# Performance work log

Measured on AMD Instinct MI355X. Metric: run time of the kernel, lower is better.

Reference implementation:

```python
import jax, jax.numpy as jnp
import numpy as np

N_NODES = 100000
N_EDGES = 3200000
D_IN = 256
D_OUT = 256


def setup_inputs() -> dict:
    key = jax.random.key(0)
    k1, k2, k3, k4, k5 = jax.random.split(key, 5)
    x = jax.random.normal(k1, (N_NODES, D_IN), dtype=jnp.float32)
    # xavier-uniform-like init for weight
    limit = float(np.sqrt(6.0 / (D_IN + D_OUT)))
    weight = jax.random.uniform(k2, (D_IN, D_OUT), dtype=jnp.float32, minval=-limit, maxval=limit)
    edge_val = jax.random.uniform(k3, (N_EDGES,), dtype=jnp.float32)
    edge_row = jax.random.randint(k4, (N_EDGES,), 0, N_NODES, dtype=jnp.int32)
    edge_col = jax.random.randint(k5, (N_EDGES,), 0, N_NODES, dtype=jnp.int32)
    return {"x": x, "weight": weight, "edge_val": edge_val,
            "edge_row": edge_row, "edge_col": edge_col}


def reference(x, weight, edge_val, edge_row, edge_col):
    # dropout p=0.0 -> identity
    support = x @ weight                                  # [N, D_OUT]
    # spmm: out[r] += val * support[c] for each edge (r, c, val)
    msgs = support[edge_col] * edge_val[:, None]          # [E, D_OUT]
    out = jax.ops.segment_sum(msgs, edge_row, num_segments=N_NODES)
    return jax.nn.relu(out)
```

## Files before the change

### kernel.cpp

```cpp
#include <hip/hip_runtime.h>

#define N_NODES 100000
#define N_EDGES 3200000
#define D 256
#define CAP 64
#define OVF_MAX 8192

#define NB1 98
#define RPB1 1024
#define CAPB1 34816
#define CHUNK 6144
#define NBLK_A ((N_EDGES + CHUNK - 1) / CHUNK)

#define CAST_BLOCKS 6250
#define GEMM_BLOCKS (N_NODES / 16)

typedef __attribute__((ext_vector_type(8))) short bf16x8;
typedef __attribute__((ext_vector_type(4))) float f32x4;

__device__ unsigned short g_wtp[(size_t)16 * 8 * 64 * 8];
__device__ int   g_cursor[N_NODES];
__device__ int   g_b1cur[NB1];
__device__ int   g_novf;
__device__ int   g_ovf_row[OVF_MAX];
__device__ int2  g_ovf_edge[OVF_MAX];

__device__ unsigned short g_xb_fb[(size_t)N_NODES * D];
__device__ unsigned       g_y_fb[(size_t)N_NODES * (D / 2)];
__device__ int2           g_pad_fb[(size_t)N_NODES * CAP];
__device__ int2           g_binned_fb[(size_t)NB1 * CAPB1];

__device__ __forceinline__ unsigned short f2bf(float f) {
    unsigned u = __float_as_uint(f);
    unsigned r = u + 0x7fffu + ((u >> 16) & 1u);
    return (unsigned short)(r >> 16);
}

__global__ void setup_kernel(const float* __restrict__ W) {
    const int tid = threadIdx.x;
    if (blockIdx.x < 64) {
        int pb = (blockIdx.x * 256 + tid) * 4;
        #pragma unroll
        for (int j = 0; j < 4; ++j) {
            int p    = pb + j;
            int i8   = p & 7;
            int lane = (p >> 3) & 63;
            int s    = (p >> 9) & 7;
            int nt   = p >> 12;
            int n = nt * 16 + (lane & 15);
            int k = s * 32 + (lane >> 4) * 8 + i8;
            g_wtp[p] = f2bf(W[(size_t)k * D + n]);
        }
    }
    if (blockIdx.x == 0) {
        if (tid < NB1) g_b1cur[tid] = 0;
        if (tid == 0) g_novf = 0;
    }
}

__launch_bounds__(256)
__global__ void binA_kernel(const float* __restrict__ edge_val,
                            const int* __restrict__ edge_row,
                            const int* __restrict__ edge_col,
                            int2* __restrict__ binned) {
    __shared__ int2 rec[CHUNK];
    __shared__ unsigned char bid[CHUNK];
    __shared__ int cnt[NB1];
    __shared__ int pre[NB1 + 1];
    __shared__ int bas[NB1];
    const int tid = threadIdx.x;
    const int e0 = blockIdx.x * CHUNK;

    for (int k = tid; k < NB1; k += 256) cnt[k] = 0;
    __syncthreads();
    #pragma unroll
    for (int j = 0; j < CHUNK / 256; ++j) {
        int e = e0 + tid + j * 256;
        if (e < N_EDGES) atomicAdd(&cnt[edge_row[e] >> 10], 1);
    }
    __syncthreads();
    if (tid == 0) {
        int run = 0;
        for (int k = 0; k < NB1; ++k) { pre[k] = run; run += cnt[k]; }
        pre[NB1] = run;
    }
    __syncthreads();
    for (int k = tid; k < NB1; k += 256)
        bas[k] = cnt[k] ? atomicAdd(&g_b1cur[k], cnt[k]) : 0;
    __syncthreads();
    for (int k = tid; k < NB1; k += 256) cnt[k] = 0;
    __syncthreads();
    #pragma unroll
    for (int j = 0; j < CHUNK / 256; ++j) {
        int e = e0 + tid + j * 256;
        if (e < N_EDGES) {
            int r = edge_row[e];
            int k = r >> 10;
            int o = atomicAdd(&cnt[k], 1);
            int pos = pre[k] + o;
            int2 pk;
            pk.x = edge_col[e] | ((r & 1023) << 17);
            pk.y = __float_as_int(edge_val[e]);
            rec[pos] = pk;
            bid[pos] = (unsigned char)k;
        }
    }
    __syncthreads();
    const int total = pre[NB1];
    for (int i = tid; i < total; i += 256) {
        int k = bid[i];
        int dest = bas[k] + (i - pre[k]);
        int2 pk = rec[i];
        if (dest < CAPB1) {
            binned[(size_t)k * CAPB1 + dest] = pk;
        } else {
            int o = atomicAdd(&g_novf, 1);
            if (o < OVF_MAX) {
                g_ovf_row[o] = (k << 10) | (pk.x >> 17);
                int2 ov; ov.x = pk.x & 0x1FFFF; ov.y = pk.y;
                g_ovf_edge[o] = ov;
            }
        }
    }
}

__launch_bounds__(256)
__global__ void binB_cast_kernel(const float* __restrict__ x,
                                 const int2* __restrict__ binned,
                                 int2* __restrict__ pad,
                                 unsigned short* __restrict__ xb) {
    __shared__ int cur[RPB1];
    const int tid = threadIdx.x;
    const int b = blockIdx.x;

    if (b < NB1) {
        for (int i = tid; i < RPB1; i += 256) cur[i] = 0;
        __syncthreads();
        const int n = min(g_b1cur[b], CAPB1);
        const int2* src = &binned[(size_t)b * CAPB1];
        for (int i = tid; i < n; i += 256) {
            int2 pk = src[i];
            int rl  = pk.x >> 17;
            int col = pk.x & 0x1FFFF;
            int slot = atomicAdd(&cur[rl], 1);
            int row = (b << 10) + rl;
            int2 o2; o2.x = col; o2.y = pk.y;
            if (slot < CAP) {
                pad[(size_t)row * CAP + slot] = o2;
            } else {
                int o = atomicAdd(&g_novf, 1);
                if (o < OVF_MAX) { g_ovf_row[o] = row; g_ovf_edge[o] = o2; }
            }
        }
        __syncthreads();
        for (int i = tid; i < RPB1; i += 256) {
            int row = (b << 10) + i;
            if (row < N_NODES) g_cursor[row] = cur[i];
        }
    } else {
        const size_t blockBase = (size_t)(b - NB1) * 4096;
        #pragma unroll
        for (int j = 0; j < 4; ++j) {
            size_t idx = blockBase + (size_t)(j * 256 + tid) * 4;
            float4 f = *(const float4*)&x[idx];
            unsigned short o[4];
            o[0] = f2bf(f.x); o[1] = f2bf(f.y);
            o[2] = f2bf(f.z); o[3] = f2bf(f.w);
            *(uint2*)&xb[idx] = *(const uint2*)o;
        }
    }
}

__launch_bounds__(128)
__global__ void spmm_kernel(const int2* __restrict__ pad,
                            const unsigned short* __restrict__ xbp,
                            unsigned* __restrict__ y) {
    const int r = blockIdx.x;
    const int t = threadIdx.x;
    const int deg = g_cursor[r];
    const int dpad = min(deg, CAP);
    const long long* rowp = (const long long*)&pad[(size_t)r * CAP];
    const unsigned* xb = (const unsigned*)xbp;

    float a0 = 0.f, a1 = 0.f;
    int i = 0;
    for (; i + 3 < dpad; i += 4) {
        long long q0 = __builtin_nontemporal_load(&rowp[i]);
        long long q1 = __builtin_nontemporal_load(&rowp[i + 1]);
        long long q2 = __builtin_nontemporal_load(&rowp[i + 2]);
        long long q3 = __builtin_nontemporal_load(&rowp[i + 3]);
        unsigned p0 = xb[(size_t)(int)q0 * (D / 2) + t];
        unsigned p1 = xb[(size_t)(int)q1 * (D / 2) + t];
        unsigned p2 = xb[(size_t)(int)q2 * (D / 2) + t];
        unsigned p3 = xb[(size_t)(int)q3 * (D / 2) + t];
        float v0 = __int_as_float((int)(q0 >> 32));
        float v1 = __int_as_float((int)(q1 >> 32));
        float v2 = __int_as_float((int)(q2 >> 32));
        float v3 = __int_as_float((int)(q3 >> 32));
        a0 += v0 * __uint_as_float(p0 << 16);
        a1 += v0 * __uint_as_float(p0 & 0xffff0000u);
        a0 += v1 * __uint_as_float(p1 << 16);
        a1 += v1 * __uint_as_float(p1 & 0xffff0000u);
        a0 += v2 * __uint_as_float(p2 << 16);
        a1 += v2 * __uint_as_float(p2 & 0xffff0000u);
        a0 += v3 * __uint_as_float(p3 << 16);
        a1 += v3 * __uint_as_float(p3 & 0xffff0000u);
    }
    for (; i < dpad; ++i) {
        long long q0 = __builtin_nontemporal_load(&rowp[i]);
        float v0 = __int_as_float((int)(q0 >> 32));
        unsigned p0 = xb[(size_t)(int)q0 * (D / 2) + t];
        a0 += v0 * __uint_as_float(p0 << 16);
        a1 += v0 * __uint_as_float(p0 & 0xffff0000u);
    }
    const int novf = min(g_novf, OVF_MAX);
    if (novf > 0) {
        for (int j = 0; j < novf; ++j) {
            if (g_ovf_row[j] == r) {
                int2 e0 = g_ovf_edge[j];
                float v0 = __int_as_float(e0.y);
                unsigned p0 = xb[(size_t)e0.x * (D / 2) + t];
                a0 += v0 * __uint_as_float(p0 << 16);
                a1 += v0 * __uint_as_float(p0 & 0xffff0000u);
            }
        }
    }
    y[(size_t)r * (D / 2) + t] =
        (unsigned)f2bf(a0) | ((unsigned)f2bf(a1) << 16);
}

__launch_bounds__(256)
__global__ void gemm_kernel(const unsigned short* __restrict__ Yb,
                            float* __restrict__ out) {
    __shared__ float tile[4][16][68];
    const int g    = blockIdx.x;
    const int wave = threadIdx.x >> 6;
    const int lane = threadIdx.x & 63;
    const int m0   = g * 16;
    const int n0   = wave * 64;
    const int lm   = lane & 15;
    const int q    = lane >> 4;

    f32x4 acc0 = {}, acc1 = {}, acc2 = {}, acc3 = {};

    #pragma unroll
    for (int s = 0; s < 8; ++s) {
        bf16x8 av = *(const bf16x8*)&Yb[(size_t)(m0 + lm) * D + s * 32 + q * 8];
        const unsigned short* bp =
            &g_wtp[((size_t)(wave * 4) * 8 + s) * 512 + lane * 8];
        bf16x8 b0 = *(const bf16x8*)&bp[0 * 4096];
        bf16x8 b1 = *(const bf16x8*)&bp[1 * 4096];
        bf16x8 b2 = *(const bf16x8*)&bp[2 * 4096];
        bf16x8 b3 = *(const bf16x8*)&bp[3 * 4096];
        acc0 = __builtin_amdgcn_mfma_f32_16x16x32_bf16(av, b0, acc0, 0, 0, 0);
        acc1 = __builtin_amdgcn_mfma_f32_16x16x32_bf16(av, b1, acc1, 0, 0, 0);
        acc2 = __builtin_amdgcn_mfma_f32_16x16x32_bf16(av, b2, acc2, 0, 0, 0);
        acc3 = __builtin_amdgcn_mfma_f32_16x16x32_bf16(av, b3, acc3, 0, 0, 0);
    }

    #pragma unroll
    for (int r = 0; r < 4; ++r) {
        tile[wave][q * 4 + r][ 0 + lm] = acc0[r];
        tile[wave][q * 4 + r][16 + lm] = acc1[r];
        tile[wave][q * 4 + r][32 + lm] = acc2[r];
        tile[wave][q * 4 + r][48 + lm] = acc3[r];
    }
    const int row  = lane >> 2;
    const int cseg = (lane & 3) * 16;
    float ov[16];
    #pragma unroll
    for (int j = 0; j < 16; ++j)
        ov[j] = fmaxf(tile[wave][row][cseg + j], 0.f);
    float* dst = &out[(size_t)(m0 + row) * D + n0 + cseg];
    #pragma unroll
    for (int j = 0; j < 4; ++j)
        __builtin_nontemporal_store(*(const f32x4*)&ov[j * 4], (f32x4*)&dst[j * 4]);
}

#define XB_BYTES   ((size_t)N_NODES * D * 2)
#define Y_BYTES    ((size_t)N_NODES * D * 2)
#define PAD_BYTES  ((size_t)N_NODES * CAP * 8)
#define BIN_BYTES  ((size_t)NB1 * CAPB1 * 8)
#define ALIGNUP(v) (((v) + 255) & ~(size_t)255)

extern "C" void kernel_launch(void* const* d_in, const int* in_sizes, int n_in,
                              void* d_out, int out_size, void* d_ws, size_t ws_size,
                              hipStream_t stream) {
    const float* x        = (const float*)d_in[0];
    const float* weight   = (const float*)d_in[1];
    const float* edge_val = (const float*)d_in[2];
    const int*   edge_row = (const int*)d_in[3];
    const int*   edge_col = (const int*)d_in[4];
    float* out = (float*)d_out;

    static void* s_xb = nullptr; static void* s_y = nullptr;
    static void* s_pad = nullptr; static void* s_bin = nullptr;
    if (!s_xb) {
        hipGetSymbolAddress(&s_xb,  HIP_SYMBOL(g_xb_fb));
        hipGetSymbolAddress(&s_y,   HIP_SYMBOL(g_y_fb));
        hipGetSymbolAddress(&s_pad, HIP_SYMBOL(g_pad_fb));
        hipGetSymbolAddress(&s_bin, HIP_SYMBOL(g_binned_fb));
    }
    unsigned short* xb;  unsigned* y;  int2* pad;  int2* binned;
    const size_t need = ALIGNUP(XB_BYTES) + ALIGNUP(Y_BYTES) +
                        ALIGNUP(PAD_BYTES) + ALIGNUP(BIN_BYTES);
    if (d_ws && ws_size >= need) {
        char* p = (char*)d_ws;
        xb     = (unsigned short*)p; p += ALIGNUP(XB_BYTES);
        y      = (unsigned*)p;       p += ALIGNUP(Y_BYTES);
        pad    = (int2*)p;           p += ALIGNUP(PAD_BYTES);
        binned = (int2*)p;
    } else {
        xb     = (unsigned short*)s_xb;
        y      = (unsigned*)s_y;
        pad    = (int2*)s_pad;
        binned = (int2*)s_bin;
    }

    setup_kernel<<<64, 256, 0, stream>>>(weight);
    binA_kernel<<<NBLK_A, 256, 0, stream>>>(edge_val, edge_row, edge_col, binned);
    binB_cast_kernel<<<NB1 + CAST_BLOCKS, 256, 0, stream>>>(x, binned, pad, xb);
    spmm_kernel<<<N_NODES, 128, 0, stream>>>(pad, xb, y);
    gemm_kernel<<<GEMM_BLOCKS, 256, 0, stream>>>((const unsigned short*)y, out);
}
```

Measured before the change: 623.6 us.

## Fuse second binning pass into SpMM via LDS-resident per-row edge lists

```diff
diff --git a/kernel.cpp b/kernel.cpp
--- a/kernel.cpp
+++ b/kernel.cpp
@@ -12,6 +12,9 @@
 #define CHUNK 6144
 #define NBLK_A ((N_EDGES + CHUNK - 1) / CHUNK)
 
+#define SLICES 8
+#define RPS 128
+
 #define CAST_BLOCKS 6250
 #define GEMM_BLOCKS (N_NODES / 16)
 
@@ -19,7 +22,6 @@
 typedef __attribute__((ext_vector_type(4))) float f32x4;
 
 __device__ unsigned short g_wtp[(size_t)16 * 8 * 64 * 8];
-__device__ int   g_cursor[N_NODES];
 __device__ int   g_b1cur[NB1];
 __device__ int   g_novf;
 __device__ int   g_ovf_row[OVF_MAX];
@@ -27,7 +29,6 @@
 
 __device__ unsigned short g_xb_fb[(size_t)N_NODES * D];
 __device__ unsigned       g_y_fb[(size_t)N_NODES * (D / 2)];
-__device__ int2           g_pad_fb[(size_t)N_NODES * CAP];
 __device__ int2           g_binned_fb[(size_t)NB1 * CAPB1];
 
 __device__ __forceinline__ unsigned short f2bf(float f) {
@@ -59,106 +60,75 @@
 }
 
 __launch_bounds__(256)
-__global__ void binA_kernel(const float* __restrict__ edge_val,
-                            const int* __restrict__ edge_row,
-                            const int* __restrict__ edge_col,
-                            int2* __restrict__ binned) {
+__global__ void binA_cast_kernel(const float* __restrict__ x,
+                                 const float* __restrict__ edge_val,
+                                 const int* __restrict__ edge_row,
+                                 const int* __restrict__ edge_col,
+                                 int2* __restrict__ binned,
+                                 unsigned short* __restrict__ xb) {
     __shared__ int2 rec[CHUNK];
     __shared__ unsigned char bid[CHUNK];
     __shared__ int cnt[NB1];
     __shared__ int pre[NB1 + 1];
     __shared__ int bas[NB1];
     const int tid = threadIdx.x;
-    const int e0 = blockIdx.x * CHUNK;
-
-    for (int k = tid; k < NB1; k += 256) cnt[k] = 0;
-    __syncthreads();
-    #pragma unroll
-    for (int j = 0; j < CHUNK / 256; ++j) {
-        int e = e0 + tid + j * 256;
-        if (e < N_EDGES) atomicAdd(&cnt[edge_row[e] >> 10], 1);
-    }
-    __syncthreads();
-    if (tid == 0) {
-        int run = 0;
-        for (int k = 0; k < NB1; ++k) { pre[k] = run; run += cnt[k]; }
-        pre[NB1] = run;
-    }
-    __syncthreads();
-    for (int k = tid; k < NB1; k += 256)
-        bas[k] = cnt[k] ? atomicAdd(&g_b1cur[k], cnt[k]) : 0;
-    __syncthreads();
-    for (int k = tid; k < NB1; k += 256) cnt[k] = 0;
-    __syncthreads();
-    #pragma unroll
-    for (int j = 0; j < CHUNK / 256; ++j) {
-        int e = e0 + tid + j * 256;
-        if (e < N_EDGES) {
-            int r = edge_row[e];
-            int k = r >> 10;
-            int o = atomicAdd(&cnt[k], 1);
-            int pos = pre[k] + o;
-            int2 pk;
-            pk.x = edge_col[e] | ((r & 1023) << 17);
-            pk.y = __float_as_int(edge_val[e]);
-            rec[pos] = pk;
-            bid[pos] = (unsigned char)k;
-        }
-    }
-    __syncthreads();
-    const int total = pre[NB1];
-    for (int i = tid; i < total; i += 256) {
-        int k = bid[i];
-        int dest = bas[k] + (i - pre[k]);
-        int2 pk = rec[i];
-        if (dest < CAPB1) {
-            binned[(size_t)k * CAPB1 + dest] = pk;
-        } else {
-            int o = atomicAdd(&g_novf, 1);
-            if (o < OVF_MAX) {
-                g_ovf_row[o] = (k << 10) | (pk.x >> 17);
-                int2 ov; ov.x = pk.x & 0x1FFFF; ov.y = pk.y;
-                g_ovf_edge[o] = ov;
+    const int b = blockIdx.x;
+
+    if (b < NBLK_A) {
+        const int e0 = b * CHUNK;
+        for (int k = tid; k < NB1; k += 256) cnt[k] = 0;
+        __syncthreads();
+        #pragma unroll
+        for (int j = 0; j < CHUNK / 256; ++j) {
+            int e = e0 + tid + j * 256;
+            if (e < N_EDGES) atomicAdd(&cnt[edge_row[e] >> 10], 1);
+        }
+        __syncthreads();
+        if (tid == 0) {
+            int run = 0;
+            for (int k = 0; k < NB1; ++k) { pre[k] = run; run += cnt[k]; }
+            pre[NB1] = run;
+        }
+        __syncthreads();
+        for (int k = tid; k < NB1; k += 256)
+            bas[k] = cnt[k] ? atomicAdd(&g_b1cur[k], cnt[k]) : 0;
+        __syncthreads();
+        for (int k = tid; k < NB1; k += 256) cnt[k] = 0;
+        __syncthreads();
+        #pragma unroll
+        for (int j = 0; j < CHUNK / 256; ++j) {
+            int e = e0 + tid + j * 256;
+            if (e < N_EDGES) {
+                int r = edge_row[e];
+                int k = r >> 10;
+                int o = atomicAdd(&cnt[k], 1);
+                int pos = pre[k] + o;
+                int2 pk;
+                pk.x = edge_col[e] | ((r & 1023) << 17);
+                pk.y = __float_as_int(edge_val[e]);
+                rec[pos] = pk;
+                bid[pos] = (unsigned char)k;
             }
         }
-    }
-}
-
-__launch_bounds__(256)
-__global__ void binB_cast_kernel(const float* __restrict__ x,
-                                 const int2* __restrict__ binned,
-                                 int2* __restrict__ pad,
-                                 unsigned short* __restrict__ xb) {
-    __shared__ int cur[RPB1];
-    const int tid = threadIdx.x;
-    const int b = blockIdx.x;
-
-    if (b < NB1) {
-        for (int i = tid; i < RPB1; i += 256) cur[i] = 0;
-        __syncthreads();
-        const int n = min(g_b1cur[b], CAPB1);
-        const int2* src = &binned[(size_t)b * CAPB1];
-        for (int i = tid; i < n; i += 256) {
-            int2 pk = src[i];
-            int rl  = pk.x >> 17;
-            int col = pk.x & 0x1FFFF;
-            int slot = atomicAdd(&cur[rl], 1);
-            int row = (b << 10) + rl;
-            int2 o2; o2.x = col; o2.y = pk.y;
-            if (slot < CAP) {
-                pad[(size_t)row * CAP + slot] = o2;
+        __syncthreads();
+        const int total = pre[NB1];
+        for (int i = tid; i < total; i += 256) {
+            int k = bid[i];
+            int dest = bas[k] + (i - pre[k]);
+            int2 pk = rec[i];
+            if (dest < CAPB1) {
+                binned[(size_t)k * CAPB1 + dest] = pk;
             } else {
                 int o = atomicAdd(&g_novf, 1);
-                if (o < OVF_MAX) { g_ovf_row[o] = row; g_ovf_edge[o] = o2; }
+                if (o < OVF_MAX) {
+                    g_ovf_row[o] = (k << 10) | (pk.x >> 17);
+                    int2 ov; ov.x = pk.x & 0x1FFFF; ov.y = pk.y;
+                    g_ovf_edge[o] = ov;
+                }
             }
         }
-        __syncthreads();
-        for (int i = tid; i < RPB1; i += 256) {
-            int row = (b << 10) + i;
-            if (row < N_NODES) g_cursor[row] = cur[i];
-        }
     } else {
-        const size_t blockBase = (size_t)(b - NB1) * 4096;
+        const size_t blockBase = (size_t)(b - NBLK_A) * 4096;
         #pragma unroll
         for (int j = 0; j < 4; ++j) {
             size_t idx = blockBase + (size_t)(j * 256 + tid) * 4;
@@ -171,62 +141,98 @@
     }
 }
 
-__launch_bounds__(128)
-__global__ void spmm_kernel(const int2* __restrict__ pad,
-                            const unsigned short* __restrict__ xbp,
-                            unsigned* __restrict__ y) {
-    const int r = blockIdx.x;
-    const int t = threadIdx.x;
-    const int deg = g_cursor[r];
-    const int dpad = min(deg, CAP);
-    const long long* rowp = (const long long*)&pad[(size_t)r * CAP];
+__launch_bounds__(256)
+__global__ void bin_spmm_kernel(const int2* __restrict__ binned,
+                                const unsigned short* __restrict__ xbp,
+                                unsigned* __restrict__ y) {
+    __shared__ int2 pad[RPS * CAP];
+    __shared__ int cur[RPS];
+    const int tid   = threadIdx.x;
+    const int bkt   = blockIdx.x >> 3;
+    const int slice = blockIdx.x & 7;
+
+    const int n = min(g_b1cur[bkt], CAPB1);
+    const int2* src = &binned[(size_t)bkt * CAPB1];
+
+    if (tid < RPS) cur[tid] = 0;
+    __syncthreads();
+    for (int i = tid; i < n; i += 256) {
+        int2 pk = src[i];
+        int rl = pk.x >> 17;
+        if ((rl >> 7) == slice) {
+            int rl7 = rl & 127;
+            int slot = atomicAdd(&cur[rl7], 1);
+            int2 o2; o2.x = pk.x & 0x1FFFF; o2.y = pk.y;
+            if (slot < CAP) {
+                pad[(rl7 << 6) + slot] = o2;
+            } else {
+                int o = atomicAdd(&g_novf, 1);
+                if (o < OVF_MAX) {
+                    g_ovf_row[o] = (bkt << 10) + (slice << 7) + rl7;
+                    g_ovf_edge[o] = o2;
+                }
+            }
+        }
+    }
+    __syncthreads();
+
+    const int grp = tid >> 7;
+    const int t   = tid & 127;
     const unsigned* xb = (const unsigned*)xbp;
-
-    float a0 = 0.f, a1 = 0.f;
-    int i = 0;
-    for (; i + 3 < dpad; i += 4) {
-        long long q0 = __builtin_nontemporal_load(&rowp[i]);
-        long long q1 = __builtin_nontemporal_load(&rowp[i + 1]);
-        long long q2 = __builtin_nontemporal_load(&rowp[i + 2]);
-        long long q3 = __builtin_nontemporal_load(&rowp[i + 3]);
-        unsigned p0 = xb[(size_t)(int)q0 * (D / 2) + t];
-        unsigned p1 = xb[(size_t)(int)q1 * (D / 2) + t];
-        unsigned p2 = xb[(size_t)(int)q2 * (D / 2) + t];
-        unsigned p3 = xb[(size_t)(int)q3 * (D / 2) + t];
-        float v0 = __int_as_float((int)(q0 >> 32));
-        float v1 = __int_as_float((int)(q1 >> 32));
-        float v2 = __int_as_float((int)(q2 >> 32));
-        float v3 = __int_as_float((int)(q3 >> 32));
-        a0 += v0 * __uint_as_float(p0 << 16);
-        a1 += v0 * __uint_as_float(p0 & 0xffff0000u);
-        a0 += v1 * __uint_as_float(p1 << 16);
-        a1 += v1 * __uint_as_float(p1 & 0xffff0000u);
-        a0 += v2 * __uint_as_float(p2 << 16);
-        a1 += v2 * __uint_as_float(p2 & 0xffff0000u);
-        a0 += v3 * __uint_as_float(p3 << 16);
-        a1 += v3 * __uint_as_float(p3 & 0xffff0000u);
-    }
-    for (; i < dpad; ++i) {
-        long long q0 = __builtin_nontemporal_load(&rowp[i]);
-        float v0 = __int_as_float((int)(q0 >> 32));
-        unsigned p0 = xb[(size_t)(int)q0 * (D / 2) + t];
-        a0 += v0 * __uint_as_float(p0 << 16);
-        a1 += v0 * __uint_as_float(p0 & 0xffff0000u);
-    }
     const int novf = min(g_novf, OVF_MAX);
-    if (novf > 0) {
-        for (int j = 0; j < novf; ++j) {
-            if (g_ovf_row[j] == r) {
-                int2 e0 = g_ovf_edge[j];
-                float v0 = __int_as_float(e0.y);
-                unsigned p0 = xb[(size_t)e0.x * (D / 2) + t];
-                a0 += v0 * __uint_as_float(p0 << 16);
-                a1 += v0 * __uint_as_float(p0 & 0xffff0000u);
+
+    for (int rp = 0; rp < RPS / 2; ++rp) {
+        const int rl7 = rp * 2 + grp;
+        const int row = (bkt << 10) + (slice << 7) + rl7;
+        if (row >= N_NODES) continue;
+        const int deg = min(cur[rl7], CAP);
+        const int2* prow = &pad[rl7 << 6];
+        float a0 = 0.f, a1 = 0.f;
+        int i = 0;
+        for (; i + 3 < deg; i += 4) {
+            int2 e0 = prow[i];
+            int2 e1 = prow[i + 1];
+            int2 e2 = prow[i + 2];
+            int2 e3 = prow[i + 3];
+            unsigned p0 = xb[(size_t)e0.x * (D / 2) + t];
+            unsigned p1 = xb[(size_t)e1.x * (D / 2) + t];
+            unsigned p2 = xb[(size_t)e2.x * (D / 2) + t];
+            unsigned p3 = xb[(size_t)e3.x * (D / 2) + t];
+            float v0 = __int_as_float(e0.y);
+            float v1 = __int_as_float(e1.y);
+            float v2 = __int_as_float(e2.y);
+            float v3 = __int_as_float(e3.y);
+            a0 += v0 * __uint_as_float(p0 << 16);
+            a1 += v0 * __uint_as_float(p0 & 0xffff0000u);
+            a0 += v1 * __uint_as_float(p1 << 16);
+            a1 += v1 * __uint_as_float(p1 & 0xffff0000u);
+            a0 += v2 * __uint_as_float(p2 << 16);
+            a1 += v2 * __uint_as_float(p2 & 0xffff0000u);
+            a0 += v3 * __uint_as_float(p3 << 16);
+            a1 += v3 * __uint_as_float(p3 & 0xffff0000u);
+        }
+        for (; i < deg; ++i) {
+            int2 e0 = prow[i];
+            unsigned p0 = xb[(size_t)e0.x * (D / 2) + t];
+            float v0 = __int_as_float(e0.y);
+            a0 += v0 * __uint_as_float(p0 << 16);
+            a1 += v0 * __uint_as_float(p0 & 0xffff0000u);
+        }
+        if (novf > 0) {
+            for (int j = 0; j < novf; ++j) {
+                if (g_ovf_row[j] == row) {
+                    int2 ee = g_ovf_edge[j];
+                    float v0 = __int_as_float(ee.y);
+                    unsigned p0 = xb[(size_t)ee.x * (D / 2) + t];
+                    a0 += v0 * __uint_as_float(p0 << 16);
+                    a1 += v0 * __uint_as_float(p0 & 0xffff0000u);
+                }
             }
         }
-    }
-    y[(size_t)r * (D / 2) + t] =
-        (unsigned)f2bf(a0) | ((unsigned)f2bf(a1) << 16);
+        __builtin_nontemporal_store(
+            (unsigned)f2bf(a0) | ((unsigned)f2bf(a1) << 16),
+            &y[(size_t)row * (D / 2) + t]);
+    }
 }
 
 __launch_bounds__(256)
@@ -279,7 +285,6 @@
 
 #define XB_BYTES   ((size_t)N_NODES * D * 2)
 #define Y_BYTES    ((size_t)N_NODES * D * 2)
-#define PAD_BYTES  ((size_t)N_NODES * CAP * 8)
 #define BIN_BYTES  ((size_t)NB1 * CAPB1 * 8)
 #define ALIGNUP(v) (((v) + 255) & ~(size_t)255)
 
@@ -294,32 +299,28 @@
     float* out = (float*)d_out;
 
     static void* s_xb = nullptr; static void* s_y = nullptr;
-    static void* s_pad = nullptr; static void* s_bin = nullptr;
+    static void* s_bin = nullptr;
     if (!s_xb) {
         hipGetSymbolAddress(&s_xb,  HIP_SYMBOL(g_xb_fb));
         hipGetSymbolAddress(&s_y,   HIP_SYMBOL(g_y_fb));
-        hipGetSymbolAddress(&s_pad, HIP_SYMBOL(g_pad_fb));
         hipGetSymbolAddress(&s_bin, HIP_SYMBOL(g_binned_fb));
     }
-    unsigned short* xb;  unsigned* y;  int2* pad;  int2* binned;
-    const size_t need = ALIGNUP(XB_BYTES) + ALIGNUP(Y_BYTES) +
-                        ALIGNUP(PAD_BYTES) + ALIGNUP(BIN_BYTES);
+    unsigned short* xb;  unsigned* y;  int2* binned;
+    const size_t need = ALIGNUP(XB_BYTES) + ALIGNUP(Y_BYTES) + ALIGNUP(BIN_BYTES);
     if (d_ws && ws_size >= need) {
         char* p = (char*)d_ws;
         xb     = (unsigned short*)p; p += ALIGNUP(XB_BYTES);
         y      = (unsigned*)p;       p += ALIGNUP(Y_BYTES);
-        pad    = (int2*)p;           p += ALIGNUP(PAD_BYTES);
         binned = (int2*)p;
     } else {
         xb     = (unsigned short*)s_xb;
         y      = (unsigned*)s_y;
-        pad    = (int2*)s_pad;
         binned = (int2*)s_bin;
     }
 
     setup_kernel<<<64, 256, 0, stream>>>(weight);
-    binA_kernel<<<NBLK_A, 256, 0, stream>>>(edge_val, edge_row, edge_col, binned);
-    binB_cast_kernel<<<NB1 + CAST_BLOCKS, 256, 0, stream>>>(x, binned, pad, xb);
-    spmm_kernel<<<N_NODES, 128, 0, stream>>>(pad, xb, y);
+    binA_cast_kernel<<<NBLK_A + CAST_BLOCKS, 256, 0, stream>>>(
+        x, edge_val, edge_row, edge_col, binned, xb);
+    bin_spmm_kernel<<<NB1 * SLICES, 256, 0, stream>>>(binned, xb, y);
     gemm_kernel<<<GEMM_BLOCKS, 256, 0, stream>>>((const unsigned short*)y, out);
 }
```

New measurement: 930.2 us. 1.49x slower.

## Replace padded per-row edge slots with compact CSR groups sorted in shared memory

Applied to the files above, without the earlier changes.

```diff
diff --git a/kernel.cpp b/kernel.cpp
--- a/kernel.cpp
+++ b/kernel.cpp
@@ -3,32 +3,35 @@
 #define N_NODES 100000
 #define N_EDGES 3200000
 #define D 256
-#define CAP 64
 #define OVF_MAX 8192
 
 #define NB1 98
-#define RPB1 1024
 #define CAPB1 34816
 #define CHUNK 6144
 #define NBLK_A ((N_EDGES + CHUNK - 1) / CHUNK)
 
+#define NQ (NB1 * 4)
+#define QROWS 256
+#define QCAP 9216
+
 #define CAST_BLOCKS 6250
 #define GEMM_BLOCKS (N_NODES / 16)
+#define SPMM_HALF 50000
 
 typedef __attribute__((ext_vector_type(8))) short bf16x8;
 typedef __attribute__((ext_vector_type(4))) float f32x4;
 
 __device__ unsigned short g_wtp[(size_t)16 * 8 * 64 * 8];
-__device__ int   g_cursor[N_NODES];
-__device__ int   g_b1cur[NB1];
+__device__ int   g_b1cur[NB1 * 16];
 __device__ int   g_novf;
 __device__ int   g_ovf_row[OVF_MAX];
 __device__ int2  g_ovf_edge[OVF_MAX];
 
 __device__ unsigned short g_xb_fb[(size_t)N_NODES * D];
 __device__ unsigned       g_y_fb[(size_t)N_NODES * (D / 2)];
-__device__ int2           g_pad_fb[(size_t)N_NODES * CAP];
 __device__ int2           g_binned_fb[(size_t)NB1 * CAPB1];
+__device__ int2           g_grp_fb[(size_t)NQ * QCAP];
+__device__ int2           g_rofs_fb[(size_t)NQ * QROWS];
 
 __device__ __forceinline__ unsigned short f2bf(float f) {
     unsigned u = __float_as_uint(f);
@@ -53,7 +56,7 @@
         }
     }
     if (blockIdx.x == 0) {
-        if (tid < NB1) g_b1cur[tid] = 0;
+        for (int i = tid; i < NB1 * 16; i += 256) g_b1cur[i] = 0;
         if (tid == 0) g_novf = 0;
     }
 }
@@ -86,7 +89,7 @@
     }
     __syncthreads();
     for (int k = tid; k < NB1; k += 256)
-        bas[k] = cnt[k] ? atomicAdd(&g_b1cur[k], cnt[k]) : 0;
+        bas[k] = cnt[k] ? atomicAdd(&g_b1cur[k * 16], cnt[k]) : 0;
     __syncthreads();
     for (int k = tid; k < NB1; k += 256) cnt[k] = 0;
     __syncthreads();
@@ -124,67 +127,98 @@
     }
 }
 
-__launch_bounds__(256)
-__global__ void binB_cast_kernel(const float* __restrict__ x,
-                                 const int2* __restrict__ binned,
-                                 int2* __restrict__ pad,
-                                 unsigned short* __restrict__ xb) {
-    __shared__ int cur[RPB1];
+__launch_bounds__(512)
+__global__ void binB_sort_kernel(const int2* __restrict__ binned,
+                                 int2* __restrict__ grp,
+                                 int2* __restrict__ rofs) {
+    __shared__ int2 srec[QCAP];
+    __shared__ int cnt[QROWS];
+    __shared__ int ofs[QROWS];
+    __shared__ int cur[QROWS];
     const int tid = threadIdx.x;
-    const int b = blockIdx.x;
-
-    if (b < NB1) {
-        for (int i = tid; i < RPB1; i += 256) cur[i] = 0;
-        __syncthreads();
-        const int n = min(g_b1cur[b], CAPB1);
-        const int2* src = &binned[(size_t)b * CAPB1];
-        for (int i = tid; i < n; i += 256) {
-            int2 pk = src[i];
-            int rl  = pk.x >> 17;
-            int col = pk.x & 0x1FFFF;
-            int slot = atomicAdd(&cur[rl], 1);
-            int row = (b << 10) + rl;
-            int2 o2; o2.x = col; o2.y = pk.y;
-            if (slot < CAP) {
-                pad[(size_t)row * CAP + slot] = o2;
+    const int b   = blockIdx.x >> 2;
+    const int qtr = blockIdx.x & 3;
+
+    const int n = min(g_b1cur[b * 16], CAPB1);
+    const int2* src = &binned[(size_t)b * CAPB1];
+
+    if (tid < QROWS) { cnt[tid] = 0; cur[tid] = 0; }
+    __syncthreads();
+    for (int i = tid; i < n; i += 512) {
+        int rl = src[i].x >> 17;
+        if ((rl >> 8) == qtr) atomicAdd(&cnt[rl & 255], 1);
+    }
+    __syncthreads();
+    if (tid < QROWS) {
+        int s = 0;
+        for (int j = 0; j < tid; ++j) s += cnt[j];
+        ofs[tid] = s;
+    }
+    __syncthreads();
+    for (int i = tid; i < n; i += 512) {
+        int2 pk = src[i];
+        int rl = pk.x >> 17;
+        if ((rl >> 8) == qtr) {
+            int r8 = rl & 255;
+            int p = ofs[r8] + atomicAdd(&cur[r8], 1);
+            int2 o2; o2.x = pk.x & 0x1FFFF; o2.y = pk.y;
+            if (p < QCAP) {
+                srec[p] = o2;
             } else {
                 int o = atomicAdd(&g_novf, 1);
-                if (o < OVF_MAX) { g_ovf_row[o] = row; g_ovf_edge[o] = o2; }
+                if (o < OVF_MAX) {
+                    g_ovf_row[o] = (b << 10) + (qtr << 8) + r8;
+                    g_ovf_edge[o] = o2;
+                }
             }
         }
-        __syncthreads();
-        for (int i = tid; i < RPB1; i += 256) {
-            int row = (b << 10) + i;
-            if (row < N_NODES) g_cursor[row] = cur[i];
-        }
-    } else {
-        const size_t blockBase = (size_t)(b - NB1) * 4096;
-        #pragma unroll
-        for (int j = 0; j < 4; ++j) {
-            size_t idx = blockBase + (size_t)(j * 256 + tid) * 4;
-            float4 f = *(const float4*)&x[idx];
-            unsigned short o[4];
-            o[0] = f2bf(f.x); o[1] = f2bf(f.y);
-            o[2] = f2bf(f.z); o[3] = f2bf(f.w);
-            *(uint2*)&xb[idx] = *(const uint2*)o;
-        }
+    }
+    __syncthreads();
+    const int total = min(ofs[QROWS - 1] + cnt[QROWS - 1], QCAP);
+    int2* dst = &grp[(size_t)blockIdx.x * QCAP];
+    for (int i = tid; i < total; i += 512) dst[i] = srec[i];
+    if (tid < QROWS) {
+        int s = min(ofs[tid], QCAP);
+        int e = min(ofs[tid] + cnt[tid], QCAP);
+        int2 oc; oc.x = s; oc.y = e - s;
+        rofs[(size_t)blockIdx.x * QROWS + tid] = oc;
+    }
+}
+
+__launch_bounds__(256)
+__global__ void cast_kernel(const float* __restrict__ x,
+                            unsigned short* __restrict__ xb) {
+    const size_t blockBase = (size_t)blockIdx.x * 4096;
+    const int tid = threadIdx.x;
+    #pragma unroll
+    for (int j = 0; j < 4; ++j) {
+        size_t idx = blockBase + (size_t)(j * 256 + tid) * 4;
+        float4 f = *(const float4*)&x[idx];
+        unsigned short o[4];
+        o[0] = f2bf(f.x); o[1] = f2bf(f.y);
+        o[2] = f2bf(f.z); o[3] = f2bf(f.w);
+        *(uint2*)&xb[idx] = *(const uint2*)o;
     }
 }
 
 __launch_bounds__(128)
-__global__ void spmm_kernel(const int2* __restrict__ pad,
+__global__ void spmm_kernel(const int2* __restrict__ grp,
+                            const int2* __restrict__ rofs,
                             const unsigned short* __restrict__ xbp,
-                            unsigned* __restrict__ y) {
-    const int r = blockIdx.x;
+                            unsigned* __restrict__ y,
+                            int rowBase) {
+    const int r = rowBase + blockIdx.x;
     const int t = threadIdx.x;
-    const int deg = g_cursor[r];
-    const int dpad = min(deg, CAP);
-    const long long* rowp = (const long long*)&pad[(size_t)r * CAP];
+    const int blk = r >> 8;
+    const int2 oc = rofs[(size_t)blk * QROWS + (r & 255)];
+    const int deg = oc.y;
+    const long long* rowp =
+        (const long long*)&grp[(size_t)blk * QCAP + oc.x];
     const unsigned* xb = (const unsigned*)xbp;
 
     float a0 = 0.f, a1 = 0.f;
     int i = 0;
-    for (; i + 3 < dpad; i += 4) {
+    for (; i + 3 < deg; i += 4) {
         long long q0 = __builtin_nontemporal_load(&rowp[i]);
         long long q1 = __builtin_nontemporal_load(&rowp[i + 1]);
         long long q2 = __builtin_nontemporal_load(&rowp[i + 2]);
@@ -206,7 +240,7 @@
         a0 += v3 * __uint_as_float(p3 << 16);
         a1 += v3 * __uint_as_float(p3 & 0xffff0000u);
     }
-    for (; i < dpad; ++i) {
+    for (; i < deg; ++i) {
         long long q0 = __builtin_nontemporal_load(&rowp[i]);
         float v0 = __int_as_float((int)(q0 >> 32));
         unsigned p0 = xb[(size_t)(int)q0 * (D / 2) + t];
@@ -279,8 +313,9 @@
 
 #define XB_BYTES   ((size_t)N_NODES * D * 2)
 #define Y_BYTES    ((size_t)N_NODES * D * 2)
-#define PAD_BYTES  ((size_t)N_NODES * CAP * 8)
 #define BIN_BYTES  ((size_t)NB1 * CAPB1 * 8)
+#define GRP_BYTES  ((size_t)NQ * QCAP * 8)
+#define ROFS_BYTES ((size_t)NQ * QROWS * 8)
 #define ALIGNUP(v) (((v) + 255) & ~(size_t)255)
 
 extern "C" void kernel_launch(void* const* d_in, const int* in_sizes, int n_in,
@@ -294,32 +329,39 @@
     float* out = (float*)d_out;
 
     static void* s_xb = nullptr; static void* s_y = nullptr;
-    static void* s_pad = nullptr; static void* s_bin = nullptr;
+    static void* s_bin = nullptr; static void* s_grp = nullptr;
+    static void* s_rofs = nullptr;
     if (!s_xb) {
-        hipGetSymbolAddress(&s_xb,  HIP_SYMBOL(g_xb_fb));
-        hipGetSymbolAddress(&s_y,   HIP_SYMBOL(g_y_fb));
-        hipGetSymbolAddress(&s_pad, HIP_SYMBOL(g_pad_fb));
-        hipGetSymbolAddress(&s_bin, HIP_SYMBOL(g_binned_fb));
-    }
-    unsigned short* xb;  unsigned* y;  int2* pad;  int2* binned;
+        hipGetSymbolAddress(&s_xb,   HIP_SYMBOL(g_xb_fb));
+        hipGetSymbolAddress(&s_y,    HIP_SYMBOL(g_y_fb));
+        hipGetSymbolAddress(&s_bin,  HIP_SYMBOL(g_binned_fb));
+        hipGetSymbolAddress(&s_grp,  HIP_SYMBOL(g_grp_fb));
+        hipGetSymbolAddress(&s_rofs, HIP_SYMBOL(g_rofs_fb));
+    }
+    unsigned short* xb;  unsigned* y;  int2* binned;  int2* grp;  int2* rofs;
     const size_t need = ALIGNUP(XB_BYTES) + ALIGNUP(Y_BYTES) +
-                        ALIGNUP(PAD_BYTES) + ALIGNUP(BIN_BYTES);
+                        ALIGNUP(BIN_BYTES) + ALIGNUP(GRP_BYTES) +
+                        ALIGNUP(ROFS_BYTES);
     if (d_ws && ws_size >= need) {
         char* p = (char*)d_ws;
         xb     = (unsigned short*)p; p += ALIGNUP(XB_BYTES);
         y      = (unsigned*)p;       p += ALIGNUP(Y_BYTES);
-        pad    = (int2*)p;           p += ALIGNUP(PAD_BYTES);
-        binned = (int2*)p;
+        binned = (int2*)p;           p += ALIGNUP(BIN_BYTES);
+        grp    = (int2*)p;           p += ALIGNUP(GRP_BYTES);
+        rofs   = (int2*)p;
     } else {
         xb     = (unsigned short*)s_xb;
         y      = (unsigned*)s_y;
-        pad    = (int2*)s_pad;
         binned = (int2*)s_bin;
+        grp    = (int2*)s_grp;
+        rofs   = (int2*)s_rofs;
     }
 
     setup_kernel<<<64, 256, 0, stream>>>(weight);
     binA_kernel<<<NBLK_A, 256, 0, stream>>>(edge_val, edge_row, edge_col, binned);
-    binB_cast_kernel<<<NB1 + CAST_BLOCKS, 256, 0, stream>>>(x, binned, pad, xb);
-    spmm_kernel<<<N_NODES, 128, 0, stream>>>(pad, xb, y);
+    binB_sort_kernel<<<NQ, 512, 0, stream>>>(binned, grp, rofs);
+    cast_kernel<<<CAST_BLOCKS, 256, 0, stream>>>(x, xb);
+    spmm_kernel<<<SPMM_HALF, 128, 0, stream>>>(grp, rofs, xb, y, 0);
+    spmm_kernel<<<SPMM_HALF, 128, 0, stream>>>(grp, rofs, xb, y, SPMM_HALF);
     gemm_kernel<<<GEMM_BLOCKS, 256, 0, stream>>>((const unsigned short*)y, out);
 }
```

Measured after the change: 620.1 us. No clear change (-0.6%).
